# Performance work log

Hardware: AMD Instinct MI355X
Metric: run time of the kernel (lower is better)

## Reference

```python
import jax, jax.numpy as jnp
import numpy as np

SIGMA = 1.0  # RBF bandwidth (kernel passed to HSIC.__init__)


def _rbf_kernel(A):
    # Gaussian RBF Gram matrix: K_ij = exp(-||a_i - a_j||^2 / (2*sigma^2))
    sq = jnp.sum(A * A, axis=1)                     # [n]
    d2 = sq[:, None] + sq[None, :] - 2.0 * (A @ A.T)  # [n, n] squared dists
    d2 = jnp.maximum(d2, 0.0)
    return jnp.exp(-d2 / (2.0 * SIGMA ** 2))


def setup_inputs() -> dict:
    key = jax.random.key(0)
    kx, ky = jax.random.split(key)
    n, d = 4096, 512
    X = jax.random.normal(kx, (n, d), dtype=jnp.float32)
    Y = jax.random.normal(ky, (n, d), dtype=jnp.float32)
    return {"X": X, "Y": Y}


def reference(X, Y):
    n = X.shape[0]
    K = _rbf_kernel(X)                      # [n, n]
    L = _rbf_kernel(Y)                      # [n, n]
    H = jnp.eye(n, dtype=X.dtype) - 1.0 / n  # centering matrix
    KH = K @ H                              # [n, n]
    LH = L @ H                              # [n, n]
    KHLH = KH @ LH                          # [n, n]
    return jnp.trace(KHLH) / (n ** 2)
```

## Files before the change

kernel.cpp:

```cpp
#include <hip/hip_runtime.h>

#define NROW 4096
#define DIM  512
#define NT   32

using short8 = __attribute__((ext_vector_type(8))) short;
using f32x4  = __attribute__((ext_vector_type(4))) float;

__device__ __forceinline__ unsigned short f2bf(float f) {
  unsigned u = __float_as_uint(f);
  u += 0x7FFFu + ((u >> 16) & 1u);
  return (unsigned short)(u >> 16);
}
__device__ __forceinline__ float bf2f(unsigned short s) {
  return __uint_as_float(((unsigned)s) << 16);
}

__global__ void __launch_bounds__(256) prep_kernel(
    const float* __restrict__ X, const float* __restrict__ Y,
    unsigned short* __restrict__ Xb, unsigned short* __restrict__ Yb,
    float* __restrict__ sqx, float* __restrict__ sqy,
    float* __restrict__ acc ) {
  int tid = threadIdx.x;
  if (blockIdx.x == 0) {
    for (int i = tid; i < 2 * NROW + 1; i += 256) acc[i] = 0.f;
  }
  int lane = tid & 63, w = tid >> 6;
  int row = blockIdx.x * 4 + w;

  {
    const float* xr = X + (size_t)row * DIM;
    unsigned short* xo = Xb + (size_t)row * DIM;
    float s = 0.f;
#pragma unroll
    for (int it = 0; it < 2; ++it) {
      int k = it * 256 + lane * 4;
      float4 v = *reinterpret_cast<const float4*>(xr + k);
      ushort4 o;
      o.x = f2bf(v.x); o.y = f2bf(v.y); o.z = f2bf(v.z); o.w = f2bf(v.w);
      float f0 = bf2f(o.x), f1 = bf2f(o.y), f2 = bf2f(o.z), f3 = bf2f(o.w);
      s += f0 * f0 + f1 * f1 + f2 * f2 + f3 * f3;
      *reinterpret_cast<ushort4*>(xo + k) = o;
    }
#pragma unroll
    for (int m = 1; m < 64; m <<= 1) s += __shfl_xor(s, m);
    if (lane == 0) sqx[row] = s;
  }
  {
    const float* yr = Y + (size_t)row * DIM;
    unsigned short* yo = Yb + (size_t)row * DIM;
    float s = 0.f;
#pragma unroll
    for (int it = 0; it < 2; ++it) {
      int k = it * 256 + lane * 4;
      float4 v = *reinterpret_cast<const float4*>(yr + k);
      ushort4 o;
      o.x = f2bf(v.x); o.y = f2bf(v.y); o.z = f2bf(v.z); o.w = f2bf(v.w);
      float f0 = bf2f(o.x), f1 = bf2f(o.y), f2 = bf2f(o.z), f3 = bf2f(o.w);
      s += f0 * f0 + f1 * f1 + f2 * f2 + f3 * f3;
      *reinterpret_cast<ushort4*>(yo + k) = o;
    }
#pragma unroll
    for (int m = 1; m < 64; m <<= 1) s += __shfl_xor(s, m);
    if (lane == 0) sqy[row] = s;
  }
}

__device__ __forceinline__ void stage_tile(unsigned short* lds,
                                           const unsigned short* gbase,
                                           int tid) {
  int w = tid >> 6;
#pragma unroll
  for (int p = 0; p < 4; ++p) {
    int q = p * 256 + tid;
    int r = q >> 3;
    int c = q & 7;
    int cs = c ^ (r & 7);
    const unsigned short* gp = gbase + r * DIM + cs * 8;
    unsigned short* lp = lds + (p * 256 + w * 64) * 8;
    __builtin_amdgcn_global_load_lds(
        (const __attribute__((address_space(1))) void*)gp,
        (__attribute__((address_space(3))) void*)lp, 16, 0, 0);
  }
}

__device__ __forceinline__ void tile_mfma(const unsigned short* At, const unsigned short* Bt,
                                          int lr, int lg, int wr, int wc,
                                          f32x4 acc[4][4]) {
#pragma unroll
  for (int kk = 0; kk < 2; ++kk) {
    short8 a[4], b[4];
#pragma unroll
    for (int m = 0; m < 4; ++m) {
      int ra = wr * 64 + m * 16 + lr;
      int ca = kk * 4 + lg;
      a[m] = *reinterpret_cast<const short8*>(At + (ra * 8 + (ca ^ (ra & 7))) * 8);
      int rb = wc * 64 + m * 16 + lr;
      b[m] = *reinterpret_cast<const short8*>(Bt + (rb * 8 + (ca ^ (rb & 7))) * 8);
    }
#pragma unroll
    for (int m = 0; m < 4; ++m)
#pragma unroll
      for (int n = 0; n < 4; ++n)
        acc[m][n] = __builtin_amdgcn_mfma_f32_16x16x32_bf16(a[m], b[n], acc[m][n], 0, 0, 0);
  }
}

__global__ void __launch_bounds__(256, 2) gram_kernel(
    const unsigned short* __restrict__ Xb, const unsigned short* __restrict__ Yb,
    const float* __restrict__ sqx, const float* __restrict__ sqy,
    float* __restrict__ rK, float* __restrict__ rL, float* __restrict__ S1) {
  __shared__ unsigned short lds[2][2][128 * 64];
  __shared__ float s1buf[4];

  int tid = threadIdx.x;
  int wg = (blockIdx.x & 7) * 66 + (blockIdx.x >> 3);
  int t = wg, bi = 0;
  while (t >= NT - bi) { t -= NT - bi; ++bi; }
  int bj = bi + t;

  int lane = tid & 63, w = tid >> 6;
  int wr = w >> 1, wc = w & 1;
  int lr = lane & 15, lg = lane >> 4;

  f32x4 accK[4][4], accL[4][4];
  f32x4 zz = {0.f, 0.f, 0.f, 0.f};
#pragma unroll
  for (int m = 0; m < 4; ++m)
#pragma unroll
    for (int n = 0; n < 4; ++n) { accK[m][n] = zz; accL[m][n] = zz; }

  const size_t rowA = (size_t)(bi * 128) * DIM;
  const size_t rowB = (size_t)(bj * 128) * DIM;

  auto stage_pair = [&](int it) {
    const unsigned short* src = (it & 8) ? Yb : Xb;
    int kb = it & 7;
    stage_tile(lds[it & 1][0], src + rowA + kb * 64, tid);
    stage_tile(lds[it & 1][1], src + rowB + kb * 64, tid);
  };

  stage_pair(0);
  __syncthreads();
#pragma unroll
  for (int kb = 0; kb < 8; ++kb) {
    stage_pair(kb + 1);
    tile_mfma(lds[kb & 1][0], lds[kb & 1][1], lr, lg, wr, wc, accK);
    __syncthreads();
  }
#pragma unroll
  for (int kb = 0; kb < 8; ++kb) {
    if (kb < 7) stage_pair(8 + kb + 1);
    tile_mfma(lds[kb & 1][0], lds[kb & 1][1], lr, lg, wr, wc, accL);
    __syncthreads();
  }

  float ckx[4] = {0.f, 0.f, 0.f, 0.f};
  float cky[4] = {0.f, 0.f, 0.f, 0.f};
  float sjx[4], sjy[4]; int gj[4];
#pragma unroll
  for (int n = 0; n < 4; ++n) {
    gj[n] = bj * 128 + wc * 64 + n * 16 + lr;
    sjx[n] = sqx[gj[n]];
    sjy[n] = sqy[gj[n]];
  }
  float s1loc = 0.f;
#pragma unroll
  for (int m = 0; m < 4; ++m) {
#pragma unroll
    for (int r = 0; r < 4; ++r) {
      int gi = bi * 128 + wr * 64 + m * 16 + lg * 4 + r;
      float six = sqx[gi], siy = sqy[gi];
      float rowk = 0.f, rowl = 0.f;
#pragma unroll
      for (int n = 0; n < 4; ++n) {
        float gk = accK[m][n][r];
        float gl = accL[m][n][r];
        float kv, lv;
        if (gi == gj[n]) {
          kv = 1.f; lv = 1.f;
        } else {
          kv = __expf(-0.5f * fmaxf(six + sjx[n] - 2.f * gk, 0.f));
          lv = __expf(-0.5f * fmaxf(siy + sjy[n] - 2.f * gl, 0.f));
        }
        s1loc += kv * lv;
        rowk += kv; rowl += lv;
        ckx[n] += kv; cky[n] += lv;
      }
#pragma unroll
      for (int msk = 1; msk < 16; msk <<= 1) {
        rowk += __shfl_xor(rowk, msk);
        rowl += __shfl_xor(rowl, msk);
      }
      if (lr == 0) { atomicAdd(&rK[gi], rowk); atomicAdd(&rL[gi], rowl); }
    }
  }
  if (bi != bj) {
#pragma unroll
    for (int n = 0; n < 4; ++n) {
      float a = ckx[n], b = cky[n];
      a += __shfl_xor(a, 16); a += __shfl_xor(a, 32);
      b += __shfl_xor(b, 16); b += __shfl_xor(b, 32);
      if (lg == 0) { atomicAdd(&rK[gj[n]], a); atomicAdd(&rL[gj[n]], b); }
    }
    s1loc *= 2.f;
  }
#pragma unroll
  for (int msk = 1; msk < 64; msk <<= 1) s1loc += __shfl_xor(s1loc, msk);
  if (lane == 0) s1buf[w] = s1loc;
  __syncthreads();
  if (tid == 0) atomicAdd(S1, s1buf[0] + s1buf[1] + s1buf[2] + s1buf[3]);
}

__global__ void __launch_bounds__(1024) finalize_kernel(
    const float* __restrict__ acc, float* __restrict__ out) {
  const float* rK = acc;
  const float* rL = acc + NROW;
  const float* S1 = acc + 2 * NROW;
  int tid = threadIdx.x, lane = tid & 63, w = tid >> 6;
  float4 a = reinterpret_cast<const float4*>(rK)[tid];
  float4 b = reinterpret_cast<const float4*>(rL)[tid];
  float sk = a.x + a.y + a.z + a.w;
  float sl = b.x + b.y + b.z + b.w;
  float s2 = a.x * b.x + a.y * b.y + a.z * b.z + a.w * b.w;
#pragma unroll
  for (int m = 1; m < 64; m <<= 1) {
    sk += __shfl_xor(sk, m);
    sl += __shfl_xor(sl, m);
    s2 += __shfl_xor(s2, m);
  }
  __shared__ float bk[16], bl[16], b2[16];
  if (lane == 0) { bk[w] = sk; bl[w] = sl; b2[w] = s2; }
  __syncthreads();
  if (tid == 0) {
    double SK = 0.0, SL = 0.0, S2 = 0.0;
#pragma unroll
    for (int i = 0; i < 16; ++i) { SK += bk[i]; SL += bl[i]; S2 += b2[i]; }
    double s1 = (double)S1[0];
    double n = (double)NROW;
    out[0] = (float)((s1 - 2.0 * S2 / n + SK * SL / (n * n)) / (n * n));
  }
}

extern "C" void kernel_launch(void* const* d_in, const int* in_sizes, int n_in,
                              void* d_out, int out_size, void* d_ws, size_t ws_size,
                              hipStream_t stream) {
  (void)in_sizes; (void)n_in; (void)out_size; (void)ws_size;
  const float* X = (const float*)d_in[0];
  const float* Y = (const float*)d_in[1];

  unsigned short* Xb = (unsigned short*)d_ws;
  unsigned short* Yb = Xb + (size_t)NROW * DIM;
  float* sqx = (float*)(Yb + (size_t)NROW * DIM);
  float* sqy = sqx + NROW;
  float* acc = sqy + NROW;

  prep_kernel<<<NROW / 4, 256, 0, stream>>>(X, Y, Xb, Yb, sqx, sqy, acc);
  gram_kernel<<<NT * (NT + 1) / 2, 256, 0, stream>>>(Xb, Yb, sqx, sqy,
                                                     acc, acc + NROW, acc + 2 * NROW);
  finalize_kernel<<<1, 1024, 0, stream>>>(acc, (float*)d_out);
}
```

Measured before the change: 116.6 us.

## Split K and L Gram tiles across two warp groups and fuse finalize via last-block

The gram kernel now runs 512 threads per block. One 256-thread group computes the X Gram tile and the other computes the Y tile concurrently, each with half the accumulator registers. The L values are exchanged through LDS (unioned with the staging buffers) so the elementwise K·L sum can be formed. The separate finalize kernel is replaced by a last-block-done atomic counter, which removes one launch. In exchange, the double-buffered prefetch is dropped in favour of a single stage with two barriers per k-step, and the block needs a larger LDS footprint for the 128x132 float exchange buffer.

```diff
diff --git a/kernel.cpp b/kernel.cpp
--- a/kernel.cpp
+++ b/kernel.cpp
@@ -23,7 +23,7 @@
     float* __restrict__ acc ) {
   int tid = threadIdx.x;
   if (blockIdx.x == 0) {
-    for (int i = tid; i < 2 * NROW + 1; i += 256) acc[i] = 0.f;
+    for (int i = tid; i < 2 * NROW + 2; i += 256) acc[i] = 0.f;
   }
   int lane = tid & 63, w = tid >> 6;
   int row = blockIdx.x * 4 + w;
@@ -68,11 +68,11 @@
 
 __device__ __forceinline__ void stage_tile(unsigned short* lds,
                                            const unsigned short* gbase,
-                                           int tid) {
-  int w = tid >> 6;
+                                           int gt) {
+  int w = gt >> 6;
 #pragma unroll
   for (int p = 0; p < 4; ++p) {
-    int q = p * 256 + tid;
+    int q = p * 256 + gt;
     int r = q >> 3;
     int c = q & 7;
     int cs = c ^ (r & 7);
@@ -85,7 +85,7 @@
 }
 
 __device__ __forceinline__ void tile_mfma(const unsigned short* At, const unsigned short* Bt,
-                                          int lr, int lg, int wr, int wc,
+                                          int lr, int lgq, int wr, int wc,
                                           f32x4 acc[4][4]) {
 #pragma unroll
   for (int kk = 0; kk < 2; ++kk) {
@@ -93,7 +93,7 @@
 #pragma unroll
     for (int m = 0; m < 4; ++m) {
       int ra = wr * 64 + m * 16 + lr;
-      int ca = kk * 4 + lg;
+      int ca = kk * 4 + lgq;
       a[m] = *reinterpret_cast<const short8*>(At + (ra * 8 + (ca ^ (ra & 7))) * 8);
       int rb = wc * 64 + m * 16 + lr;
       b[m] = *reinterpret_cast<const short8*>(Bt + (rb * 8 + (ca ^ (rb & 7))) * 8);
@@ -106,139 +106,150 @@
   }
 }
 
-__global__ void __launch_bounds__(256, 2) gram_kernel(
+__global__ void __launch_bounds__(512, 4) gram_kernel(
     const unsigned short* __restrict__ Xb, const unsigned short* __restrict__ Yb,
     const float* __restrict__ sqx, const float* __restrict__ sqy,
-    float* __restrict__ rK, float* __restrict__ rL, float* __restrict__ S1) {
-  __shared__ unsigned short lds[2][2][128 * 64];
+    float* __restrict__ accbuf, float* __restrict__ out) {
+  __shared__ union SM {
+    unsigned short stage[2][2][128 * 64];
+    float lx[128 * 132];
+  } sm;
   __shared__ float s1buf[4];
+  __shared__ int lastf;
+  __shared__ float fin[3][8];
+
+  float* rKg = accbuf;
+  float* rLg = accbuf + NROW;
+  float* S1g = accbuf + 2 * NROW;
+  unsigned int* cnt = (unsigned int*)(accbuf + 2 * NROW + 1);
 
   int tid = threadIdx.x;
+  int g    = tid >> 8;
+  int gt   = tid & 255;
+  int lane = tid & 63;
+  int gw   = (tid >> 6) & 3;
+  int wr = gw >> 1, wc = gw & 1;
+  int lr = lane & 15, lgq = lane >> 4;
+
   int wg = (blockIdx.x & 7) * 66 + (blockIdx.x >> 3);
   int t = wg, bi = 0;
   while (t >= NT - bi) { t -= NT - bi; ++bi; }
   int bj = bi + t;
 
-  int lane = tid & 63, w = tid >> 6;
-  int wr = w >> 1, wc = w & 1;
-  int lr = lane & 15, lg = lane >> 4;
-
-  f32x4 accK[4][4], accL[4][4];
-  f32x4 zz = {0.f, 0.f, 0.f, 0.f};
-#pragma unroll
-  for (int m = 0; m < 4; ++m)
-#pragma unroll
-    for (int n = 0; n < 4; ++n) { accK[m][n] = zz; accL[m][n] = zz; }
-
+  const unsigned short* src = g ? Yb : Xb;
+  const float* sq = g ? sqy : sqx;
+  float* racc = g ? rLg : rKg;
+
+  unsigned short* tA = sm.stage[g][0];
+  unsigned short* tB = sm.stage[g][1];
   const size_t rowA = (size_t)(bi * 128) * DIM;
   const size_t rowB = (size_t)(bj * 128) * DIM;
 
-  auto stage_pair = [&](int it) {
-    const unsigned short* src = (it & 8) ? Yb : Xb;
-    int kb = it & 7;
-    stage_tile(lds[it & 1][0], src + rowA + kb * 64, tid);
-    stage_tile(lds[it & 1][1], src + rowB + kb * 64, tid);
-  };
-
-  stage_pair(0);
-  __syncthreads();
-#pragma unroll
+  f32x4 acc[4][4];
+  f32x4 zz = {0.f, 0.f, 0.f, 0.f};
+#pragma unroll
+  for (int m = 0; m < 4; ++m)
+#pragma unroll
+    for (int n = 0; n < 4; ++n) acc[m][n] = zz;
+
   for (int kb = 0; kb < 8; ++kb) {
-    stage_pair(kb + 1);
-    tile_mfma(lds[kb & 1][0], lds[kb & 1][1], lr, lg, wr, wc, accK);
+    stage_tile(tA, src + rowA + kb * 64, gt);
+    stage_tile(tB, src + rowB + kb * 64, gt);
     __syncthreads();
-  }
-#pragma unroll
-  for (int kb = 0; kb < 8; ++kb) {
-    if (kb < 7) stage_pair(8 + kb + 1);
-    tile_mfma(lds[kb & 1][0], lds[kb & 1][1], lr, lg, wr, wc, accL);
+    tile_mfma(tA, tB, lr, lgq, wr, wc, acc);
     __syncthreads();
   }
 
-  float ckx[4] = {0.f, 0.f, 0.f, 0.f};
-  float cky[4] = {0.f, 0.f, 0.f, 0.f};
-  float sjx[4], sjy[4]; int gj[4];
+  float colsum[4] = {0.f, 0.f, 0.f, 0.f};
+  int cj[4]; float sj[4];
 #pragma unroll
   for (int n = 0; n < 4; ++n) {
-    gj[n] = bj * 128 + wc * 64 + n * 16 + lr;
-    sjx[n] = sqx[gj[n]];
-    sjy[n] = sqy[gj[n]];
-  }
-  float s1loc = 0.f;
+    cj[n] = wc * 64 + n * 16 + lr;
+    sj[n] = sq[bj * 128 + cj[n]];
+  }
 #pragma unroll
   for (int m = 0; m < 4; ++m) {
 #pragma unroll
     for (int r = 0; r < 4; ++r) {
-      int gi = bi * 128 + wr * 64 + m * 16 + lg * 4 + r;
-      float six = sqx[gi], siy = sqy[gi];
-      float rowk = 0.f, rowl = 0.f;
+      int ri = wr * 64 + m * 16 + lgq * 4 + r;
+      float si = sq[bi * 128 + ri];
+      float rowsum = 0.f;
 #pragma unroll
       for (int n = 0; n < 4; ++n) {
-        float gk = accK[m][n][r];
-        float gl = accL[m][n][r];
-        float kv, lv;
-        if (gi == gj[n]) {
-          kv = 1.f; lv = 1.f;
-        } else {
-          kv = __expf(-0.5f * fmaxf(six + sjx[n] - 2.f * gk, 0.f));
-          lv = __expf(-0.5f * fmaxf(siy + sjy[n] - 2.f * gl, 0.f));
-        }
-        s1loc += kv * lv;
-        rowk += kv; rowl += lv;
-        ckx[n] += kv; cky[n] += lv;
+        float d = acc[m][n][r];
+        float v;
+        if (bi * 128 + ri == bj * 128 + cj[n]) v = 1.f;
+        else v = __expf(-0.5f * fmaxf(si + sj[n] - 2.f * d, 0.f));
+        acc[m][n][r] = v;
+        rowsum += v; colsum[n] += v;
+        if (g) sm.lx[ri * 132 + cj[n]] = v;
       }
 #pragma unroll
-      for (int msk = 1; msk < 16; msk <<= 1) {
-        rowk += __shfl_xor(rowk, msk);
-        rowl += __shfl_xor(rowl, msk);
+      for (int msk = 1; msk < 16; msk <<= 1) rowsum += __shfl_xor(rowsum, msk);
+      if (lr == 0) atomicAdd(&racc[bi * 128 + ri], rowsum);
+    }
+  }
+  if (bi != bj) {
+#pragma unroll
+    for (int n = 0; n < 4; ++n) {
+      float a = colsum[n];
+      a += __shfl_xor(a, 16); a += __shfl_xor(a, 32);
+      if (lgq == 0) atomicAdd(&racc[bj * 128 + cj[n]], a);
+    }
+  }
+
+  __syncthreads();
+
+  if (g == 0) {
+    float s1 = 0.f;
+#pragma unroll
+    for (int m = 0; m < 4; ++m)
+#pragma unroll
+      for (int r = 0; r < 4; ++r) {
+        int ri = wr * 64 + m * 16 + lgq * 4 + r;
+#pragma unroll
+        for (int n = 0; n < 4; ++n)
+          s1 += acc[m][n][r] * sm.lx[ri * 132 + cj[n]];
       }
-      if (lr == 0) { atomicAdd(&rK[gi], rowk); atomicAdd(&rL[gi], rowl); }
-    }
-  }
-  if (bi != bj) {
-#pragma unroll
-    for (int n = 0; n < 4; ++n) {
-      float a = ckx[n], b = cky[n];
-      a += __shfl_xor(a, 16); a += __shfl_xor(a, 32);
-      b += __shfl_xor(b, 16); b += __shfl_xor(b, 32);
-      if (lg == 0) { atomicAdd(&rK[gj[n]], a); atomicAdd(&rL[gj[n]], b); }
-    }
-    s1loc *= 2.f;
-  }
-#pragma unroll
-  for (int msk = 1; msk < 64; msk <<= 1) s1loc += __shfl_xor(s1loc, msk);
-  if (lane == 0) s1buf[w] = s1loc;
-  __syncthreads();
-  if (tid == 0) atomicAdd(S1, s1buf[0] + s1buf[1] + s1buf[2] + s1buf[3]);
-}
-
-__global__ void __launch_bounds__(1024) finalize_kernel(
-    const float* __restrict__ acc, float* __restrict__ out) {
-  const float* rK = acc;
-  const float* rL = acc + NROW;
-  const float* S1 = acc + 2 * NROW;
-  int tid = threadIdx.x, lane = tid & 63, w = tid >> 6;
-  float4 a = reinterpret_cast<const float4*>(rK)[tid];
-  float4 b = reinterpret_cast<const float4*>(rL)[tid];
-  float sk = a.x + a.y + a.z + a.w;
-  float sl = b.x + b.y + b.z + b.w;
-  float s2 = a.x * b.x + a.y * b.y + a.z * b.z + a.w * b.w;
-#pragma unroll
-  for (int m = 1; m < 64; m <<= 1) {
-    sk += __shfl_xor(sk, m);
-    sl += __shfl_xor(sl, m);
-    s2 += __shfl_xor(s2, m);
-  }
-  __shared__ float bk[16], bl[16], b2[16];
-  if (lane == 0) { bk[w] = sk; bl[w] = sl; b2[w] = s2; }
+    if (bi != bj) s1 *= 2.f;
+#pragma unroll
+    for (int msk = 1; msk < 64; msk <<= 1) s1 += __shfl_xor(s1, msk);
+    if (lane == 0) s1buf[gw] = s1;
+  }
+  __syncthreads();
+  if (tid == 0) atomicAdd(S1g, s1buf[0] + s1buf[1] + s1buf[2] + s1buf[3]);
+
+  __threadfence();
+  __syncthreads();
+  if (tid == 0) lastf = (atomicAdd(cnt, 1u) == (unsigned)(NT * (NT + 1) / 2 - 1));
+  __syncthreads();
+  if (!lastf) return;
+
+  __threadfence();
+  float sk = 0.f, sl = 0.f, s2 = 0.f;
+  int base = tid * 8;
+#pragma unroll
+  for (int i = 0; i < 8; ++i) {
+    float a = __hip_atomic_load(rKg + base + i, __ATOMIC_RELAXED, __HIP_MEMORY_SCOPE_AGENT);
+    float b = __hip_atomic_load(rLg + base + i, __ATOMIC_RELAXED, __HIP_MEMORY_SCOPE_AGENT);
+    sk += a; sl += b; s2 += a * b;
+  }
+#pragma unroll
+  for (int msk = 1; msk < 64; msk <<= 1) {
+    sk += __shfl_xor(sk, msk);
+    sl += __shfl_xor(sl, msk);
+    s2 += __shfl_xor(s2, msk);
+  }
+  int w8 = tid >> 6;
+  if (lane == 0) { fin[0][w8] = sk; fin[1][w8] = sl; fin[2][w8] = s2; }
   __syncthreads();
   if (tid == 0) {
     double SK = 0.0, SL = 0.0, S2 = 0.0;
 #pragma unroll
-    for (int i = 0; i < 16; ++i) { SK += bk[i]; SL += bl[i]; S2 += b2[i]; }
-    double s1 = (double)S1[0];
+    for (int i = 0; i < 8; ++i) { SK += fin[0][i]; SL += fin[1][i]; S2 += fin[2][i]; }
+    double s1v = (double)__hip_atomic_load(S1g, __ATOMIC_RELAXED, __HIP_MEMORY_SCOPE_AGENT);
     double n = (double)NROW;
-    out[0] = (float)((s1 - 2.0 * S2 / n + SK * SL / (n * n)) / (n * n));
+    out[0] = (float)((s1v - 2.0 * S2 / n + SK * SL / (n * n)) / (n * n));
   }
 }
 
@@ -256,7 +267,6 @@
   float* acc = sqy + NROW;
 
   prep_kernel<<<NROW / 4, 256, 0, stream>>>(X, Y, Xb, Yb, sqx, sqy, acc);
-  gram_kernel<<<NT * (NT + 1) / 2, 256, 0, stream>>>(Xb, Yb, sqx, sqy,
-                                                     acc, acc + NROW, acc + 2 * NROW);
-  finalize_kernel<<<1, 1024, 0, stream>>>(acc, (float*)d_out);
-}
+  gram_kernel<<<NT * (NT + 1) / 2, 512, 0, stream>>>(Xb, Yb, sqx, sqy,
+                                                     acc, (float*)d_out);
+}
```

Result: slower. 174.3 us (+49.5%).

## Quantize inputs to FP8 for Gram MFMAs and fuse finalize via last-block reduction

Applied to the files above, without the earlier changes.

Converts X and Y to FP8 e4m3 instead of bf16 and runs the Gram products with fp8 16x16x32 MFMAs. The K dimension per stage doubles in elements for the same bytes, and the LDS swizzle is reworked for 8-byte fragments. The separate finalize kernel is removed: the last block to finish, found with an atomic counter, performs the final reduction, saving one launch. FP8 quantization of random normal data adds sizeable error to the squared distances that feed exp, so accuracy may fail tolerance.

```diff
diff --git a/kernel.cpp b/kernel.cpp
--- a/kernel.cpp
+++ b/kernel.cpp
@@ -1,46 +1,37 @@
 #include <hip/hip_runtime.h>
+#include <hip/hip_fp8.h>
 
 #define NROW 4096
 #define DIM  512
 #define NT   32
 
-using short8 = __attribute__((ext_vector_type(8))) short;
-using f32x4  = __attribute__((ext_vector_type(4))) float;
-
-__device__ __forceinline__ unsigned short f2bf(float f) {
-  unsigned u = __float_as_uint(f);
-  u += 0x7FFFu + ((u >> 16) & 1u);
-  return (unsigned short)(u >> 16);
-}
-__device__ __forceinline__ float bf2f(unsigned short s) {
-  return __uint_as_float(((unsigned)s) << 16);
-}
+using f32x4 = __attribute__((ext_vector_type(4))) float;
 
 __global__ void __launch_bounds__(256) prep_kernel(
     const float* __restrict__ X, const float* __restrict__ Y,
-    unsigned short* __restrict__ Xb, unsigned short* __restrict__ Yb,
+    unsigned char* __restrict__ Xq, unsigned char* __restrict__ Yq,
     float* __restrict__ sqx, float* __restrict__ sqy,
     float* __restrict__ acc ) {
   int tid = threadIdx.x;
   if (blockIdx.x == 0) {
-    for (int i = tid; i < 2 * NROW + 1; i += 256) acc[i] = 0.f;
+    for (int i = tid; i < 2 * NROW + 2; i += 256) acc[i] = 0.f;
   }
   int lane = tid & 63, w = tid >> 6;
   int row = blockIdx.x * 4 + w;
 
   {
     const float* xr = X + (size_t)row * DIM;
-    unsigned short* xo = Xb + (size_t)row * DIM;
+    unsigned char* xo = Xq + (size_t)row * DIM;
     float s = 0.f;
 #pragma unroll
     for (int it = 0; it < 2; ++it) {
       int k = it * 256 + lane * 4;
       float4 v = *reinterpret_cast<const float4*>(xr + k);
-      ushort4 o;
-      o.x = f2bf(v.x); o.y = f2bf(v.y); o.z = f2bf(v.z); o.w = f2bf(v.w);
-      float f0 = bf2f(o.x), f1 = bf2f(o.y), f2 = bf2f(o.z), f3 = bf2f(o.w);
+      __hip_fp8_e4m3 q0(v.x), q1(v.y), q2(v.z), q3(v.w);
+      uchar4 o = make_uchar4(q0.__x, q1.__x, q2.__x, q3.__x);
+      float f0 = (float)q0, f1 = (float)q1, f2 = (float)q2, f3 = (float)q3;
       s += f0 * f0 + f1 * f1 + f2 * f2 + f3 * f3;
-      *reinterpret_cast<ushort4*>(xo + k) = o;
+      *reinterpret_cast<uchar4*>(xo + k) = o;
     }
 #pragma unroll
     for (int m = 1; m < 64; m <<= 1) s += __shfl_xor(s, m);
@@ -48,17 +39,17 @@
   }
   {
     const float* yr = Y + (size_t)row * DIM;
-    unsigned short* yo = Yb + (size_t)row * DIM;
+    unsigned char* yo = Yq + (size_t)row * DIM;
     float s = 0.f;
 #pragma unroll
     for (int it = 0; it < 2; ++it) {
       int k = it * 256 + lane * 4;
       float4 v = *reinterpret_cast<const float4*>(yr + k);
-      ushort4 o;
-      o.x = f2bf(v.x); o.y = f2bf(v.y); o.z = f2bf(v.z); o.w = f2bf(v.w);
-      float f0 = bf2f(o.x), f1 = bf2f(o.y), f2 = bf2f(o.z), f3 = bf2f(o.w);
+      __hip_fp8_e4m3 q0(v.x), q1(v.y), q2(v.z), q3(v.w);
+      uchar4 o = make_uchar4(q0.__x, q1.__x, q2.__x, q3.__x);
+      float f0 = (float)q0, f1 = (float)q1, f2 = (float)q2, f3 = (float)q3;
       s += f0 * f0 + f1 * f1 + f2 * f2 + f3 * f3;
-      *reinterpret_cast<ushort4*>(yo + k) = o;
+      *reinterpret_cast<uchar4*>(yo + k) = o;
     }
 #pragma unroll
     for (int m = 1; m < 64; m <<= 1) s += __shfl_xor(s, m);
@@ -66,52 +57,60 @@
   }
 }
 
-__device__ __forceinline__ void stage_tile(unsigned short* lds,
-                                           const unsigned short* gbase,
+__device__ __forceinline__ void stage_tile(unsigned char* lds,
+                                           const unsigned char* gbase,
                                            int tid) {
   int w = tid >> 6;
 #pragma unroll
-  for (int p = 0; p < 4; ++p) {
+  for (int p = 0; p < 2; ++p) {
     int q = p * 256 + tid;
-    int r = q >> 3;
-    int c = q & 7;
-    int cs = c ^ (r & 7);
-    const unsigned short* gp = gbase + r * DIM + cs * 8;
-    unsigned short* lp = lds + (p * 256 + w * 64) * 8;
+    int r = q >> 2;
+    int c = q & 3;
+    int cs = c ^ (r & 3);
+    const unsigned char* gp = gbase + r * DIM + cs * 16;
+    unsigned char* lp = lds + (p * 256 + w * 64) * 16;
     __builtin_amdgcn_global_load_lds(
         (const __attribute__((address_space(1))) void*)gp,
         (__attribute__((address_space(3))) void*)lp, 16, 0, 0);
   }
 }
 
-__device__ __forceinline__ void tile_mfma(const unsigned short* At, const unsigned short* Bt,
-                                          int lr, int lg, int wr, int wc,
+__device__ __forceinline__ void tile_mfma(const unsigned char* At, const unsigned char* Bt,
+                                          int lr, int lgq, int wr, int wc,
                                           f32x4 acc[4][4]) {
 #pragma unroll
   for (int kk = 0; kk < 2; ++kk) {
-    short8 a[4], b[4];
+    long a[4], b[4];
+    int ca8 = kk * 4 + lgq;
+    int cc = ca8 >> 1, h = ca8 & 1;
 #pragma unroll
     for (int m = 0; m < 4; ++m) {
       int ra = wr * 64 + m * 16 + lr;
-      int ca = kk * 4 + lg;
-      a[m] = *reinterpret_cast<const short8*>(At + (ra * 8 + (ca ^ (ra & 7))) * 8);
+      a[m] = *reinterpret_cast<const long*>(At + ra * 64 + ((cc ^ (ra & 3)) << 4) + (h << 3));
       int rb = wc * 64 + m * 16 + lr;
-      b[m] = *reinterpret_cast<const short8*>(Bt + (rb * 8 + (ca ^ (rb & 7))) * 8);
+      b[m] = *reinterpret_cast<const long*>(Bt + rb * 64 + ((cc ^ (rb & 3)) << 4) + (h << 3));
     }
 #pragma unroll
     for (int m = 0; m < 4; ++m)
 #pragma unroll
       for (int n = 0; n < 4; ++n)
-        acc[m][n] = __builtin_amdgcn_mfma_f32_16x16x32_bf16(a[m], b[n], acc[m][n], 0, 0, 0);
+        acc[m][n] = __builtin_amdgcn_mfma_f32_16x16x32_fp8_fp8(a[m], b[n], acc[m][n], 0, 0, 0);
   }
 }
 
 __global__ void __launch_bounds__(256, 2) gram_kernel(
-    const unsigned short* __restrict__ Xb, const unsigned short* __restrict__ Yb,
+    const unsigned char* __restrict__ Xq, const unsigned char* __restrict__ Yq,
     const float* __restrict__ sqx, const float* __restrict__ sqy,
-    float* __restrict__ rK, float* __restrict__ rL, float* __restrict__ S1) {
-  __shared__ unsigned short lds[2][2][128 * 64];
+    float* __restrict__ accbuf, float* __restrict__ out) {
+  __shared__ unsigned char lds[2][2][128 * 64];
   __shared__ float s1buf[4];
+  __shared__ int lastf;
+  __shared__ float fin[3][4];
+
+  float* rK = accbuf;
+  float* rL = accbuf + NROW;
+  float* S1 = accbuf + 2 * NROW;
+  unsigned int* cnt = (unsigned int*)(accbuf + 2 * NROW + 1);
 
   int tid = threadIdx.x;
   int wg = (blockIdx.x & 7) * 66 + (blockIdx.x >> 3);
@@ -121,7 +120,7 @@
 
   int lane = tid & 63, w = tid >> 6;
   int wr = w >> 1, wc = w & 1;
-  int lr = lane & 15, lg = lane >> 4;
+  int lr = lane & 15, lgq = lane >> 4;
 
   f32x4 accK[4][4], accL[4][4];
   f32x4 zz = {0.f, 0.f, 0.f, 0.f};
@@ -134,7 +133,7 @@
   const size_t rowB = (size_t)(bj * 128) * DIM;
 
   auto stage_pair = [&](int it) {
-    const unsigned short* src = (it & 8) ? Yb : Xb;
+    const unsigned char* src = (it & 8) ? Yq : Xq;
     int kb = it & 7;
     stage_tile(lds[it & 1][0], src + rowA + kb * 64, tid);
     stage_tile(lds[it & 1][1], src + rowB + kb * 64, tid);
@@ -145,13 +144,13 @@
 #pragma unroll
   for (int kb = 0; kb < 8; ++kb) {
     stage_pair(kb + 1);
-    tile_mfma(lds[kb & 1][0], lds[kb & 1][1], lr, lg, wr, wc, accK);
+    tile_mfma(lds[kb & 1][0], lds[kb & 1][1], lr, lgq, wr, wc, accK);
     __syncthreads();
   }
 #pragma unroll
   for (int kb = 0; kb < 8; ++kb) {
     if (kb < 7) stage_pair(8 + kb + 1);
-    tile_mfma(lds[kb & 1][0], lds[kb & 1][1], lr, lg, wr, wc, accL);
+    tile_mfma(lds[kb & 1][0], lds[kb & 1][1], lr, lgq, wr, wc, accL);
     __syncthreads();
   }
 
@@ -169,7 +168,7 @@
   for (int m = 0; m < 4; ++m) {
 #pragma unroll
     for (int r = 0; r < 4; ++r) {
-      int gi = bi * 128 + wr * 64 + m * 16 + lg * 4 + r;
+      int gi = bi * 128 + wr * 64 + m * 16 + lgq * 4 + r;
       float six = sqx[gi], siy = sqy[gi];
       float rowk = 0.f, rowl = 0.f;
 #pragma unroll
@@ -177,9 +176,8 @@
         float gk = accK[m][n][r];
         float gl = accL[m][n][r];
         float kv, lv;
-        if (gi == gj[n]) {
-          kv = 1.f; lv = 1.f;
-        } else {
+        if (gi == gj[n]) { kv = 1.f; lv = 1.f; }
+        else {
           kv = __expf(-0.5f * fmaxf(six + sjx[n] - 2.f * gk, 0.f));
           lv = __expf(-0.5f * fmaxf(siy + sjy[n] - 2.f * gl, 0.f));
         }
@@ -201,7 +199,7 @@
       float a = ckx[n], b = cky[n];
       a += __shfl_xor(a, 16); a += __shfl_xor(a, 32);
       b += __shfl_xor(b, 16); b += __shfl_xor(b, 32);
-      if (lg == 0) { atomicAdd(&rK[gj[n]], a); atomicAdd(&rL[gj[n]], b); }
+      if (lgq == 0) { atomicAdd(&rK[gj[n]], a); atomicAdd(&rL[gj[n]], b); }
     }
     s1loc *= 2.f;
   }
@@ -210,35 +208,37 @@
   if (lane == 0) s1buf[w] = s1loc;
   __syncthreads();
   if (tid == 0) atomicAdd(S1, s1buf[0] + s1buf[1] + s1buf[2] + s1buf[3]);
-}
-
-__global__ void __launch_bounds__(1024) finalize_kernel(
-    const float* __restrict__ acc, float* __restrict__ out) {
-  const float* rK = acc;
-  const float* rL = acc + NROW;
-  const float* S1 = acc + 2 * NROW;
-  int tid = threadIdx.x, lane = tid & 63, w = tid >> 6;
-  float4 a = reinterpret_cast<const float4*>(rK)[tid];
-  float4 b = reinterpret_cast<const float4*>(rL)[tid];
-  float sk = a.x + a.y + a.z + a.w;
-  float sl = b.x + b.y + b.z + b.w;
-  float s2 = a.x * b.x + a.y * b.y + a.z * b.z + a.w * b.w;
-#pragma unroll
-  for (int m = 1; m < 64; m <<= 1) {
-    sk += __shfl_xor(sk, m);
-    sl += __shfl_xor(sl, m);
-    s2 += __shfl_xor(s2, m);
-  }
-  __shared__ float bk[16], bl[16], b2[16];
-  if (lane == 0) { bk[w] = sk; bl[w] = sl; b2[w] = s2; }
+
+  __threadfence();
+  __syncthreads();
+  if (tid == 0) lastf = (atomicAdd(cnt, 1u) == (unsigned)(NT * (NT + 1) / 2 - 1));
+  __syncthreads();
+  if (!lastf) return;
+
+  __threadfence();
+  float sk = 0.f, sl = 0.f, s2 = 0.f;
+  int base = tid * 16;
+#pragma unroll
+  for (int i = 0; i < 16; ++i) {
+    float a = __hip_atomic_load(rK + base + i, __ATOMIC_RELAXED, __HIP_MEMORY_SCOPE_AGENT);
+    float b = __hip_atomic_load(rL + base + i, __ATOMIC_RELAXED, __HIP_MEMORY_SCOPE_AGENT);
+    sk += a; sl += b; s2 += a * b;
+  }
+#pragma unroll
+  for (int msk = 1; msk < 64; msk <<= 1) {
+    sk += __shfl_xor(sk, msk);
+    sl += __shfl_xor(sl, msk);
+    s2 += __shfl_xor(s2, msk);
+  }
+  if (lane == 0) { fin[0][w] = sk; fin[1][w] = sl; fin[2][w] = s2; }
   __syncthreads();
   if (tid == 0) {
     double SK = 0.0, SL = 0.0, S2 = 0.0;
 #pragma unroll
-    for (int i = 0; i < 16; ++i) { SK += bk[i]; SL += bl[i]; S2 += b2[i]; }
-    double s1 = (double)S1[0];
+    for (int i = 0; i < 4; ++i) { SK += fin[0][i]; SL += fin[1][i]; S2 += fin[2][i]; }
+    double s1v = (double)__hip_atomic_load(S1, __ATOMIC_RELAXED, __HIP_MEMORY_SCOPE_AGENT);
     double n = (double)NROW;
-    out[0] = (float)((s1 - 2.0 * S2 / n + SK * SL / (n * n)) / (n * n));
+    out[0] = (float)((s1v - 2.0 * S2 / n + SK * SL / (n * n)) / (n * n));
   }
 }
 
@@ -249,14 +249,13 @@
   const float* X = (const float*)d_in[0];
   const float* Y = (const float*)d_in[1];
 
-  unsigned short* Xb = (unsigned short*)d_ws;
-  unsigned short* Yb = Xb + (size_t)NROW * DIM;
-  float* sqx = (float*)(Yb + (size_t)NROW * DIM);
+  unsigned char* Xq = (unsigned char*)d_ws;
+  unsigned char* Yq = Xq + (size_t)NROW * DIM;
+  float* sqx = (float*)(Yq + (size_t)NROW * DIM);
   float* sqy = sqx + NROW;
   float* acc = sqy + NROW;
 
-  prep_kernel<<<NROW / 4, 256, 0, stream>>>(X, Y, Xb, Yb, sqx, sqy, acc);
-  gram_kernel<<<NT * (NT + 1) / 2, 256, 0, stream>>>(Xb, Yb, sqx, sqy,
-                                                     acc, acc + NROW, acc + 2 * NROW);
-  finalize_kernel<<<1, 1024, 0, stream>>>(acc, (float*)d_out);
-}
+  prep_kernel<<<NROW / 4, 256, 0, stream>>>(X, Y, Xq, Yq, sqx, sqy, acc);
+  gram_kernel<<<NT * (NT + 1) / 2, 256, 0, stream>>>(Xq, Yq, sqx, sqy,
+                                                     acc, (float*)d_out);
+}
```

New measurement: 148.8 us. 1.28x slower.

## Process two tile pairs per block, pipeline loads with vmcnt waits, fuse finalize

Applied to the files above, without the earlier changes.

The grid is halved so each block computes two upper-triangular tile pairs in sequence, filling roughly one wave of blocks on the GPU. The K-loop merges the X and Y phases into one 16-step double-buffered pipeline that uses explicit vmcnt waits and raw s_barrier in place of full __syncthreads. The separate finalize kernel is replaced by a last-block-done counter that runs the final reduction inside the gram kernel, saving one launch. The risks are that fewer blocks give less latency hiding and that the tail work is serialized in the last block.

```diff
diff --git a/kernel.cpp b/kernel.cpp
--- a/kernel.cpp
+++ b/kernel.cpp
@@ -3,6 +3,8 @@
 #define NROW 4096
 #define DIM  512
 #define NT   32
+#define NPAIR 528
+#define NBLK  264
 
 using short8 = __attribute__((ext_vector_type(8))) short;
 using f32x4  = __attribute__((ext_vector_type(4))) float;
@@ -23,7 +25,7 @@
     float* __restrict__ acc ) {
   int tid = threadIdx.x;
   if (blockIdx.x == 0) {
-    for (int i = tid; i < 2 * NROW + 1; i += 256) acc[i] = 0.f;
+    for (int i = tid; i < 2 * NROW + 2; i += 256) acc[i] = 0.f;
   }
   int lane = tid & 63, w = tid >> 6;
   int row = blockIdx.x * 4 + w;
@@ -85,7 +87,7 @@
 }
 
 __device__ __forceinline__ void tile_mfma(const unsigned short* At, const unsigned short* Bt,
-                                          int lr, int lg, int wr, int wc,
+                                          int lr, int lgq, int wr, int wc,
                                           f32x4 acc[4][4]) {
 #pragma unroll
   for (int kk = 0; kk < 2; ++kk) {
@@ -93,7 +95,7 @@
 #pragma unroll
     for (int m = 0; m < 4; ++m) {
       int ra = wr * 64 + m * 16 + lr;
-      int ca = kk * 4 + lg;
+      int ca = kk * 4 + lgq;
       a[m] = *reinterpret_cast<const short8*>(At + (ra * 8 + (ca ^ (ra & 7))) * 8);
       int rb = wc * 64 + m * 16 + lr;
       b[m] = *reinterpret_cast<const short8*>(Bt + (rb * 8 + (ca ^ (rb & 7))) * 8);
@@ -109,136 +111,148 @@
 __global__ void __launch_bounds__(256, 2) gram_kernel(
     const unsigned short* __restrict__ Xb, const unsigned short* __restrict__ Yb,
     const float* __restrict__ sqx, const float* __restrict__ sqy,
-    float* __restrict__ rK, float* __restrict__ rL, float* __restrict__ S1) {
+    float* __restrict__ accbuf, float* __restrict__ out) {
   __shared__ unsigned short lds[2][2][128 * 64];
   __shared__ float s1buf[4];
+  __shared__ int lastf;
+  __shared__ float fin[3][4];
+
+  float* rK = accbuf;
+  float* rL = accbuf + NROW;
+  float* S1 = accbuf + 2 * NROW;
+  unsigned int* cnt = (unsigned int*)(accbuf + 2 * NROW + 1);
 
   int tid = threadIdx.x;
-  int wg = (blockIdx.x & 7) * 66 + (blockIdx.x >> 3);
-  int t = wg, bi = 0;
-  while (t >= NT - bi) { t -= NT - bi; ++bi; }
-  int bj = bi + t;
-
   int lane = tid & 63, w = tid >> 6;
   int wr = w >> 1, wc = w & 1;
-  int lr = lane & 15, lg = lane >> 4;
-
-  f32x4 accK[4][4], accL[4][4];
-  f32x4 zz = {0.f, 0.f, 0.f, 0.f};
-#pragma unroll
-  for (int m = 0; m < 4; ++m)
-#pragma unroll
-    for (int n = 0; n < 4; ++n) { accK[m][n] = zz; accL[m][n] = zz; }
-
-  const size_t rowA = (size_t)(bi * 128) * DIM;
-  const size_t rowB = (size_t)(bj * 128) * DIM;
-
-  auto stage_pair = [&](int it) {
-    const unsigned short* src = (it & 8) ? Yb : Xb;
-    int kb = it & 7;
-    stage_tile(lds[it & 1][0], src + rowA + kb * 64, tid);
-    stage_tile(lds[it & 1][1], src + rowB + kb * 64, tid);
-  };
-
-  stage_pair(0);
+  int lr = lane & 15, lgq = lane >> 4;
+
+  int wg = (blockIdx.x & 7) * 33 + (blockIdx.x >> 3);
+
+  for (int pp = 0; pp < 2; ++pp) {
+    int t = wg * 2 + pp, bi = 0;
+    while (t >= NT - bi) { t -= NT - bi; ++bi; }
+    int bj = bi + t;
+
+    f32x4 accK[4][4], accL[4][4];
+    f32x4 zz = {0.f, 0.f, 0.f, 0.f};
+#pragma unroll
+    for (int m = 0; m < 4; ++m)
+#pragma unroll
+      for (int n = 0; n < 4; ++n) { accK[m][n] = zz; accL[m][n] = zz; }
+
+    const size_t rowA = (size_t)(bi * 128) * DIM;
+    const size_t rowB = (size_t)(bj * 128) * DIM;
+
+    auto stage_pair = [&](int it) {
+      const unsigned short* src = (it & 8) ? Yb : Xb;
+      int kb = it & 7;
+      stage_tile(lds[it & 1][0], src + rowA + kb * 64, tid);
+      stage_tile(lds[it & 1][1], src + rowB + kb * 64, tid);
+    };
+
+    stage_pair(0);
+#pragma unroll
+    for (int st = 0; st < 16; ++st) {
+      if (st < 15) {
+        stage_pair(st + 1);
+        asm volatile("s_waitcnt vmcnt(8)" ::: "memory");
+      } else {
+        asm volatile("s_waitcnt vmcnt(0)" ::: "memory");
+      }
+      __builtin_amdgcn_s_barrier();
+      __builtin_amdgcn_sched_barrier(0);
+      tile_mfma(lds[st & 1][0], lds[st & 1][1], lr, lgq, wr, wc,
+                (st < 8) ? accK : accL);
+      __builtin_amdgcn_s_barrier();
+    }
+
+    float ckx[4] = {0.f, 0.f, 0.f, 0.f};
+    float cky[4] = {0.f, 0.f, 0.f, 0.f};
+    float sjx[4], sjy[4]; int gj[4];
+#pragma unroll
+    for (int n = 0; n < 4; ++n) {
+      gj[n] = bj * 128 + wc * 64 + n * 16 + lr;
+      sjx[n] = sqx[gj[n]];
+      sjy[n] = sqy[gj[n]];
+    }
+    float s1loc = 0.f;
+#pragma unroll
+    for (int m = 0; m < 4; ++m) {
+#pragma unroll
+      for (int r = 0; r < 4; ++r) {
+        int gi = bi * 128 + wr * 64 + m * 16 + lgq * 4 + r;
+        float six = sqx[gi], siy = sqy[gi];
+        float rowk = 0.f, rowl = 0.f;
+#pragma unroll
+        for (int n = 0; n < 4; ++n) {
+          float gk = accK[m][n][r];
+          float gl = accL[m][n][r];
+          float kv, lv;
+          if (gi == gj[n]) { kv = 1.f; lv = 1.f; }
+          else {
+            kv = __expf(-0.5f * fmaxf(six + sjx[n] - 2.f * gk, 0.f));
+            lv = __expf(-0.5f * fmaxf(siy + sjy[n] - 2.f * gl, 0.f));
+          }
+          s1loc += kv * lv;
+          rowk += kv; rowl += lv;
+          ckx[n] += kv; cky[n] += lv;
+        }
+#pragma unroll
+        for (int msk = 1; msk < 16; msk <<= 1) {
+          rowk += __shfl_xor(rowk, msk);
+          rowl += __shfl_xor(rowl, msk);
+        }
+        if (lr == 0) { atomicAdd(&rK[gi], rowk); atomicAdd(&rL[gi], rowl); }
+      }
+    }
+    if (bi != bj) {
+#pragma unroll
+      for (int n = 0; n < 4; ++n) {
+        float a = ckx[n], b = cky[n];
+        a += __shfl_xor(a, 16); a += __shfl_xor(a, 32);
+        b += __shfl_xor(b, 16); b += __shfl_xor(b, 32);
+        if (lgq == 0) { atomicAdd(&rK[gj[n]], a); atomicAdd(&rL[gj[n]], b); }
+      }
+      s1loc *= 2.f;
+    }
+#pragma unroll
+    for (int msk = 1; msk < 64; msk <<= 1) s1loc += __shfl_xor(s1loc, msk);
+    if (lane == 0) s1buf[w] = s1loc;
+    __syncthreads();
+    if (tid == 0) atomicAdd(S1, s1buf[0] + s1buf[1] + s1buf[2] + s1buf[3]);
+  }
+
+  __threadfence();
   __syncthreads();
-#pragma unroll
-  for (int kb = 0; kb < 8; ++kb) {
-    stage_pair(kb + 1);
-    tile_mfma(lds[kb & 1][0], lds[kb & 1][1], lr, lg, wr, wc, accK);
-    __syncthreads();
-  }
-#pragma unroll
-  for (int kb = 0; kb < 8; ++kb) {
-    if (kb < 7) stage_pair(8 + kb + 1);
-    tile_mfma(lds[kb & 1][0], lds[kb & 1][1], lr, lg, wr, wc, accL);
-    __syncthreads();
-  }
-
-  float ckx[4] = {0.f, 0.f, 0.f, 0.f};
-  float cky[4] = {0.f, 0.f, 0.f, 0.f};
-  float sjx[4], sjy[4]; int gj[4];
-#pragma unroll
-  for (int n = 0; n < 4; ++n) {
-    gj[n] = bj * 128 + wc * 64 + n * 16 + lr;
-    sjx[n] = sqx[gj[n]];
-    sjy[n] = sqy[gj[n]];
-  }
-  float s1loc = 0.f;
-#pragma unroll
-  for (int m = 0; m < 4; ++m) {
-#pragma unroll
-    for (int r = 0; r < 4; ++r) {
-      int gi = bi * 128 + wr * 64 + m * 16 + lg * 4 + r;
-      float six = sqx[gi], siy = sqy[gi];
-      float rowk = 0.f, rowl = 0.f;
-#pragma unroll
-      for (int n = 0; n < 4; ++n) {
-        float gk = accK[m][n][r];
-        float gl = accL[m][n][r];
-        float kv, lv;
-        if (gi == gj[n]) {
-          kv = 1.f; lv = 1.f;
-        } else {
-          kv = __expf(-0.5f * fmaxf(six + sjx[n] - 2.f * gk, 0.f));
-          lv = __expf(-0.5f * fmaxf(siy + sjy[n] - 2.f * gl, 0.f));
-        }
-        s1loc += kv * lv;
-        rowk += kv; rowl += lv;
-        ckx[n] += kv; cky[n] += lv;
-      }
-#pragma unroll
-      for (int msk = 1; msk < 16; msk <<= 1) {
-        rowk += __shfl_xor(rowk, msk);
-        rowl += __shfl_xor(rowl, msk);
-      }
-      if (lr == 0) { atomicAdd(&rK[gi], rowk); atomicAdd(&rL[gi], rowl); }
-    }
-  }
-  if (bi != bj) {
-#pragma unroll
-    for (int n = 0; n < 4; ++n) {
-      float a = ckx[n], b = cky[n];
-      a += __shfl_xor(a, 16); a += __shfl_xor(a, 32);
-      b += __shfl_xor(b, 16); b += __shfl_xor(b, 32);
-      if (lg == 0) { atomicAdd(&rK[gj[n]], a); atomicAdd(&rL[gj[n]], b); }
-    }
-    s1loc *= 2.f;
-  }
-#pragma unroll
-  for (int msk = 1; msk < 64; msk <<= 1) s1loc += __shfl_xor(s1loc, msk);
-  if (lane == 0) s1buf[w] = s1loc;
+  if (tid == 0) lastf = (atomicAdd(cnt, 1u) == (unsigned)(NBLK - 1));
   __syncthreads();
-  if (tid == 0) atomicAdd(S1, s1buf[0] + s1buf[1] + s1buf[2] + s1buf[3]);
-}
-
-__global__ void __launch_bounds__(1024) finalize_kernel(
-    const float* __restrict__ acc, float* __restrict__ out) {
-  const float* rK = acc;
-  const float* rL = acc + NROW;
-  const float* S1 = acc + 2 * NROW;
-  int tid = threadIdx.x, lane = tid & 63, w = tid >> 6;
-  float4 a = reinterpret_cast<const float4*>(rK)[tid];
-  float4 b = reinterpret_cast<const float4*>(rL)[tid];
-  float sk = a.x + a.y + a.z + a.w;
-  float sl = b.x + b.y + b.z + b.w;
-  float s2 = a.x * b.x + a.y * b.y + a.z * b.z + a.w * b.w;
-#pragma unroll
-  for (int m = 1; m < 64; m <<= 1) {
-    sk += __shfl_xor(sk, m);
-    sl += __shfl_xor(sl, m);
-    s2 += __shfl_xor(s2, m);
-  }
-  __shared__ float bk[16], bl[16], b2[16];
-  if (lane == 0) { bk[w] = sk; bl[w] = sl; b2[w] = s2; }
+  if (!lastf) return;
+
+  __threadfence();
+  float sk = 0.f, sl = 0.f, s2 = 0.f;
+  int base = tid * 16;
+#pragma unroll
+  for (int i = 0; i < 16; ++i) {
+    float a = __hip_atomic_load(rK + base + i, __ATOMIC_RELAXED, __HIP_MEMORY_SCOPE_AGENT);
+    float b = __hip_atomic_load(rL + base + i, __ATOMIC_RELAXED, __HIP_MEMORY_SCOPE_AGENT);
+    sk += a; sl += b; s2 += a * b;
+  }
+#pragma unroll
+  for (int msk = 1; msk < 64; msk <<= 1) {
+    sk += __shfl_xor(sk, msk);
+    sl += __shfl_xor(sl, msk);
+    s2 += __shfl_xor(s2, msk);
+  }
+  if (lane == 0) { fin[0][w] = sk; fin[1][w] = sl; fin[2][w] = s2; }
   __syncthreads();
   if (tid == 0) {
     double SK = 0.0, SL = 0.0, S2 = 0.0;
 #pragma unroll
-    for (int i = 0; i < 16; ++i) { SK += bk[i]; SL += bl[i]; S2 += b2[i]; }
-    double s1 = (double)S1[0];
+    for (int i = 0; i < 4; ++i) { SK += fin[0][i]; SL += fin[1][i]; S2 += fin[2][i]; }
+    double s1v = (double)__hip_atomic_load(S1, __ATOMIC_RELAXED, __HIP_MEMORY_SCOPE_AGENT);
     double n = (double)NROW;
-    out[0] = (float)((s1 - 2.0 * S2 / n + SK * SL / (n * n)) / (n * n));
+    out[0] = (float)((s1v - 2.0 * S2 / n + SK * SL / (n * n)) / (n * n));
   }
 }
 
@@ -256,7 +270,5 @@
   float* acc = sqy + NROW;
 
   prep_kernel<<<NROW / 4, 256, 0, stream>>>(X, Y, Xb, Yb, sqx, sqy, acc);
-  gram_kernel<<<NT * (NT + 1) / 2, 256, 0, stream>>>(Xb, Yb, sqx, sqy,
-                                                     acc, acc + NROW, acc + 2 * NROW);
-  finalize_kernel<<<1, 1024, 0, stream>>>(acc, (float*)d_out);
-}
+  gram_kernel<<<NBLK, 256, 0, stream>>>(Xb, Yb, sqx, sqy, acc, (float*)d_out);
+}
```

Measured after the change: 134.8 us. 1.16x slower.
